# Performance work log

Measured on AMD Instinct MI355X. Metric: run time of the kernel, lower is better.

Reference implementation:

```python
import jax, jax.numpy as jnp
import numpy as np

B, S1, S2, H = 8, 2048, 2048, 1024

def setup_inputs() -> dict:
    key = jax.random.key(0)
    k1, k2, kw, kb = jax.random.split(key, 4)
    hidden1 = jax.random.normal(k1, (B, S1, H), dtype=jnp.float32)
    hidden2 = jax.random.normal(k2, (B, S2, H), dtype=jnp.float32)
    W = jax.random.normal(kw, (H, H), dtype=jnp.float32) * 0.001
    bias = jax.random.normal(kb, (1,), dtype=jnp.float32) * 0.02
    return {"hidden1": hidden1, "hidden2": hidden2, "W": W, "bias": bias}

def reference(hidden1, hidden2, W, bias):
    # weight[b, i, j] = (hidden1 @ W)[b, i, :] . hidden2[b, j, :] + bias
    weight = jnp.einsum('bih,hk,bjk->bij', hidden1, W, hidden2) + bias[0]  # (B, S1, S2)
    # softmax over s1 (dim=1), then transpose-bmm with hidden1 -> (B, S2, H)
    a1 = jax.nn.softmax(weight, axis=1)
    hidden_1 = jnp.einsum('bij,bih->bjh', a1, hidden1)
    # softmax over s2 (dim=2), bmm with hidden2 -> (B, S1, H)
    a2 = jax.nn.softmax(weight, axis=2)
    hidden_2 = jnp.einsum('bij,bjh->bih', a2, hidden2)
    return (hidden_1, hidden_2)
```

## Files before the change

kernel.cpp:

```cpp
#include <hip/hip_runtime.h>
#include <stdint.h>

#define B_  8
#define S1_ 2048
#define S2_ 2048
#define H_  1024

typedef __attribute__((ext_vector_type(8))) short bf16x8;
typedef __attribute__((ext_vector_type(4))) float f32x4;
typedef unsigned short u16;

__device__ __forceinline__ u16 f2bf(float f){
  union { float f; uint32_t v; } x; x.f = f;
  uint32_t r = x.v + 0x7fffu + ((x.v >> 16) & 1u);
  return (u16)(r >> 16);
}
__device__ __forceinline__ u16 f2h(float f){
  union { _Float16 h; u16 u; } c; c.h = (_Float16)f; return c.u;
}
__device__ __forceinline__ float h2f(u16 u){
  union { _Float16 h; u16 u; } c; c.u = u; return (float)c.h;
}
__device__ __forceinline__ uint32_t pk2bf(float lo, float hi){
  uint32_t r;
  asm("v_cvt_pk_bf16_f32 %0, %1, %2" : "=v"(r) : "v"(lo), "v"(hi));
  return r;
}
__device__ __forceinline__ void async16(void* lds, const void* g){
  __builtin_amdgcn_global_load_lds(
      (const __attribute__((address_space(1))) uint32_t*)g,
      (__attribute__((address_space(3))) uint32_t*)lds, 16, 0, 0);
}

__global__ __launch_bounds__(256) void k_cvt_bf16(const float* __restrict__ in,
                                                  u16* __restrict__ out, long n){
  long i = ((long)blockIdx.x * 256 + threadIdx.x) * 8;
  const long stride = (long)gridDim.x * 256 * 8;
  for (; i < n; i += stride){
    float4 a = *(const float4*)(in + i);
    float4 b = *(const float4*)(in + i + 4);
    union { bf16x8 v; uint32_t w[4]; } o;
    o.w[0] = pk2bf(a.x, a.y); o.w[1] = pk2bf(a.z, a.w);
    o.w[2] = pk2bf(b.x, b.y); o.w[3] = pk2bf(b.z, b.w);
    *(bf16x8*)(out + i) = o.v;
  }
}

__global__ __launch_bounds__(256) void k_tcvt(const float* __restrict__ in,
                                              u16* __restrict__ out, int R, int Cc){
  __shared__ u16 t[32][33];
  in  += (long)blockIdx.z * R * Cc;
  out += (long)blockIdx.z * R * Cc;
  const int x = threadIdx.x & 31, y0 = threadIdx.x >> 5;
  const int bx = blockIdx.x * 32, by = blockIdx.y * 32;
  for (int r = y0; r < 32; r += 8) t[r][x] = f2bf(in[(long)(by + r) * Cc + bx + x]);
  __syncthreads();
  for (int r = y0; r < 32; r += 8) out[(long)(bx + r) * R + by + x] = t[x][r];
}

__global__ __launch_bounds__(256) void k_cvtT(const float* __restrict__ in,
                                              u16* __restrict__ out_n,
                                              u16* __restrict__ out_t, int R, int Cc){
  __shared__ u16 t[32][33];
  in   += (long)blockIdx.z * R * Cc;
  out_n += (long)blockIdx.z * R * Cc;
  out_t += (long)blockIdx.z * R * Cc;
  const int x = threadIdx.x & 31, y0 = threadIdx.x >> 5;
  const int bx = blockIdx.x * 32, by = blockIdx.y * 32;
  for (int r = y0; r < 32; r += 8){
    u16 bv = f2bf(in[(long)(by + r) * Cc + bx + x]);
    out_n[(long)(by + r) * Cc + bx + x] = bv;
    t[r][x] = bv;
  }
  __syncthreads();
  for (int r = y0; r < 32; r += 8) out_t[(long)(bx + r) * R + by + x] = t[x][r];
}

template<int OM, bool STATS>
__global__ __launch_bounds__(512) void k_gemm256(
    const u16* __restrict__ A, const u16* __restrict__ Bm, void* __restrict__ Cv,
    int M, int N, int K, long sA, long sB, long sC,
    float* __restrict__ rpmax, float* __restrict__ rpsum,
    float* __restrict__ cpmax, float* __restrict__ cpsum)
{
  A += (long)blockIdx.z * sA; Bm += (long)blockIdx.z * sB;
  __shared__ u16 lds[4 * 16384];
  const int tid = threadIdx.x, lane = tid & 63, w = tid >> 6;
  const int wm = w >> 2, wn = w & 3;
  const int brow = blockIdx.x * 256, bcol = blockIdx.y * 256;

  f32x4 acc[8][4];
#pragma unroll
  for (int m=0;m<8;++m)
#pragma unroll
    for (int n=0;n<4;++n) acc[m][n] = (f32x4){0.f,0.f,0.f,0.f};

  const int fr = lane & 15;
  const int g8s = ((lane >> 4) ^ ((lane >> 1) & 3)) * 8;

  const int cc0 = w*128 + lane;
  const int cc1 = w*128 + 64 + lane;
  const int sl0 = (cc0 & 3) ^ ((cc0 >> 3) & 3);
  const int sl1 = (cc1 & 3) ^ ((cc1 >> 3) & 3);
  const u16* gA0 = A  + (long)(brow + (cc0 >> 2)) * K + sl0*8;
  const u16* gA1 = A  + (long)(brow + (cc1 >> 2)) * K + sl1*8;
  const u16* gB0 = Bm + (long)(bcol + (cc0 >> 2)) * K + sl0*8;
  const u16* gB1 = Bm + (long)(bcol + (cc1 >> 2)) * K + sl1*8;
  const int ldA0 = (w*128)*8, ldA1 = (w*128 + 64)*8;

  auto stage = [&](int buf, int t){
    u16* base = lds + buf*16384;
    async16(base + ldA0,        gA0 + t*32);
    async16(base + ldA1,        gA1 + t*32);
    async16(base + 8192 + ldA0, gB0 + t*32);
    async16(base + 8192 + ldA1, gB1 + t*32);
  };
  auto ldfrag = [&](int buf, bf16x8* a, bf16x8* b){
    const u16* At = lds + buf*16384;
    const u16* Bt = At + 8192;
#pragma unroll
    for (int n=0;n<4;++n) b[n] = *(const bf16x8*)(Bt + (wn*64 + n*16 + fr)*32 + g8s);
#pragma unroll
    for (int m=0;m<8;++m) a[m] = *(const bf16x8*)(At + (wm*128 + m*16 + fr)*32 + g8s);
  };

  const int NT = K >> 5;
  stage(0,0); stage(1,1); stage(2,2);
  asm volatile("s_waitcnt vmcnt(4)" ::: "memory");
  __builtin_amdgcn_s_barrier();

  bf16x8 a0[8], b0[4], a1[8], b1[4];
  ldfrag(0, a0, b0);

  for (int t = 0; t < NT; t += 2){
    if (t + 3 < NT) stage((t+3)&3, t+3);
    ldfrag((t+1)&3, a1, b1);
    __builtin_amdgcn_sched_barrier(0);
    __builtin_amdgcn_s_setprio(1);
#pragma unroll
    for (int m=0;m<8;++m)
#pragma unroll
      for (int n=0;n<4;++n)
        acc[m][n] = __builtin_amdgcn_mfma_f32_16x16x32_bf16(a0[m], b0[n], acc[m][n], 0,0,0);
    __builtin_amdgcn_s_setprio(0);
    asm volatile("s_waitcnt vmcnt(4)" ::: "memory");
    __builtin_amdgcn_s_barrier();

    if (t + 4 < NT) stage((t+4)&3, t+4);
    if (t + 2 < NT) ldfrag((t+2)&3, a0, b0);
    __builtin_amdgcn_sched_barrier(0);
    __builtin_amdgcn_s_setprio(1);
#pragma unroll
    for (int m=0;m<8;++m)
#pragma unroll
      for (int n=0;n<4;++n)
        acc[m][n] = __builtin_amdgcn_mfma_f32_16x16x32_bf16(a1[m], b1[n], acc[m][n], 0,0,0);
    __builtin_amdgcn_s_setprio(0);
    if (t + 2 < NT){
      asm volatile("s_waitcnt vmcnt(4)" ::: "memory");
      __builtin_amdgcn_s_barrier();
    }
  }

  const int crow = brow + wm*128 + (lane >> 4) * 4;
  const int ccol = bcol + wn*64 + fr;
  if constexpr (OM == 2){
    float* C = (float*)Cv + (long)blockIdx.z * sC;
#pragma unroll
    for (int m=0;m<8;++m)
#pragma unroll
      for (int n=0;n<4;++n){
        f32x4 v = acc[m][n];
        float* cp = C + (long)(crow + m*16) * N + ccol + n*16;
#pragma unroll
        for (int q=0;q<4;++q) cp[(long)q*N] = v[q];
      }
  } else {
    u16* C = (u16*)Cv + (long)blockIdx.z * sC;
#pragma unroll
    for (int m=0;m<8;++m)
#pragma unroll
      for (int n=0;n<4;++n){
        f32x4 v = acc[m][n];
        u16* cp = C + (long)(crow + m*16) * N + ccol + n*16;
#pragma unroll
        for (int q=0;q<4;++q) cp[(long)q*N] = OM ? f2h(v[q]) : f2bf(v[q]);
      }
  }

  if constexpr (STATS){
    const int hi = lane >> 4;
#pragma unroll
    for (int m=0;m<8;++m){
      f32x4 mx = acc[m][0];
#pragma unroll
      for (int n=1;n<4;++n)
#pragma unroll
        for (int q=0;q<4;++q) mx[q] = fmaxf(mx[q], acc[m][n][q]);
#pragma unroll
      for (int off=1; off<16; off<<=1)
#pragma unroll
        for (int q=0;q<4;++q) mx[q] = fmaxf(mx[q], __shfl_xor(mx[q], off));
      f32x4 sm = (f32x4){0.f,0.f,0.f,0.f};
#pragma unroll
      for (int n=0;n<4;++n)
#pragma unroll
        for (int q=0;q<4;++q) sm[q] += __expf(acc[m][n][q] - mx[q]);
#pragma unroll
      for (int off=1; off<16; off<<=1)
#pragma unroll
        for (int q=0;q<4;++q) sm[q] += __shfl_xor(sm[q], off);
      if (fr == 0){
        const int nb = blockIdx.y*4 + wn;
        const long rb = ((long)blockIdx.z*32 + nb)*2048 + brow + wm*128 + m*16 + hi*4;
#pragma unroll
        for (int q=0;q<4;++q){ rpmax[rb+q] = mx[q]; rpsum[rb+q] = sm[q]; }
      }
    }
#pragma unroll
    for (int n=0;n<4;++n){
      float mx = acc[0][n][0];
#pragma unroll
      for (int m=0;m<8;++m)
#pragma unroll
        for (int q=0;q<4;++q) mx = fmaxf(mx, acc[m][n][q]);
      mx = fmaxf(mx, __shfl_xor(mx, 16));
      mx = fmaxf(mx, __shfl_xor(mx, 32));
      float sm = 0.f;
#pragma unroll
      for (int m=0;m<8;++m)
#pragma unroll
        for (int q=0;q<4;++q) sm += __expf(acc[m][n][q] - mx);
      sm += __shfl_xor(sm, 16);
      sm += __shfl_xor(sm, 32);
      if (hi == 0){
        const int mb = blockIdx.x*2 + wm;
        const long cb = ((long)blockIdx.z*16 + mb)*2048 + bcol + wn*64 + n*16 + fr;
        cpmax[cb] = mx; cpsum[cb] = sm;
      }
    }
  }
}

__global__ __launch_bounds__(256) void k_combine(
    const float* __restrict__ rpmax, const float* __restrict__ rpsum,
    const float* __restrict__ cpmax, const float* __restrict__ cpsum,
    float* __restrict__ rmax, float* __restrict__ rinv,
    float* __restrict__ cmax, float* __restrict__ cinv)
{
  const long i = (long)blockIdx.x*256 + threadIdx.x;
  const int b = (int)(i >> 11), r = (int)(i & 2047);
  if (blockIdx.y == 0){
    const float* pm = rpmax + ((long)b*32)*2048 + r;
    const float* ps = rpsum + ((long)b*32)*2048 + r;
    float m = -3.4e38f;
#pragma unroll
    for (int k=0;k<32;++k) m = fmaxf(m, pm[(long)k*2048]);
    float s = 0.f;
#pragma unroll
    for (int k=0;k<32;++k) s += ps[(long)k*2048] * __expf(pm[(long)k*2048] - m);
    rmax[i] = m; rinv[i] = 1.f / s;
  } else {
    const float* pm = cpmax + ((long)b*16)*2048 + r;
    const float* ps = cpsum + ((long)b*16)*2048 + r;
    float m = -3.4e38f;
#pragma unroll
    for (int k=0;k<16;++k) m = fmaxf(m, pm[(long)k*2048]);
    float s = 0.f;
#pragma unroll
    for (int k=0;k<16;++k) s += ps[(long)k*2048] * __expf(pm[(long)k*2048] - m);
    cmax[i] = m; cinv[i] = 1.f / s;
  }
}

__global__ __launch_bounds__(256) void k_p1t(u16* __restrict__ Wg, u16* __restrict__ P2,
                                             const float* __restrict__ cmax,
                                             const float* __restrict__ cinv,
                                             const float* __restrict__ rmax,
                                             const float* __restrict__ rinv){
  const int ti = blockIdx.x, tj = blockIdx.y;
  if (tj < ti) return;
  const int b = blockIdx.z;
  u16* S = Wg + (long)b * S1_ * S2_;
  const int jl = threadIdx.x & 63, ig = threadIdx.x >> 6;
  const int I0 = ti*64, J0 = tj*64;
  const float cmA = cmax[b*S2_ + J0 + jl], ciA = cinv[b*S2_ + J0 + jl];
  const float cmB = cmax[b*S2_ + I0 + jl], ciB = cinv[b*S2_ + I0 + jl];
  float ra[16], rc[16];
#pragma unroll
  for (int q=0;q<16;++q) ra[q] = h2f(S[(long)(I0 + ig*16 + q)*S2_ + J0 + jl]);
#pragma unroll
  for (int q=0;q<16;++q) rc[q] = h2f(S[(long)(J0 + ig*16 + q)*S2_ + I0 + jl]);

  if (P2){
    u16* P2b = P2 + (long)b * S1_ * S2_;
#pragma unroll
    for (int q=0;q<16;++q){
      const int r = I0 + ig*16 + q;
      P2b[(long)r*S2_ + J0 + jl] = f2bf(__expf(ra[q] - rmax[b*S1_+r]) * rinv[b*S1_+r]);
    }
    if (ti != tj){
#pragma unroll
      for (int q=0;q<16;++q){
        const int r = J0 + ig*16 + q;
        P2b[(long)r*S2_ + I0 + jl] = f2bf(__expf(rc[q] - rmax[b*S1_+r]) * rinv[b*S1_+r]);
      }
    }
  }

  float a[16], c[16];
#pragma unroll
  for (int q=0;q<16;++q) a[q] = __expf(ra[q] - cmA) * ciA;
#pragma unroll
  for (int q=0;q<16;++q) c[q] = __expf(rc[q] - cmB) * ciB;
  __syncthreads();
  union { bf16x8 v; uint32_t w4[4]; } o0, o1;
#pragma unroll
  for (int k=0;k<4;++k){ o0.w4[k] = pk2bf(a[2*k], a[2*k+1]); o1.w4[k] = pk2bf(a[8+2*k], a[9+2*k]); }
  *(bf16x8*)(S + (long)(J0+jl)*S2_ + I0 + ig*16)     = o0.v;
  *(bf16x8*)(S + (long)(J0+jl)*S2_ + I0 + ig*16 + 8) = o1.v;
#pragma unroll
  for (int k=0;k<4;++k){ o0.w4[k] = pk2bf(c[2*k], c[2*k+1]); o1.w4[k] = pk2bf(c[8+2*k], c[9+2*k]); }
  *(bf16x8*)(S + (long)(I0+jl)*S2_ + J0 + ig*16)     = o0.v;
  *(bf16x8*)(S + (long)(I0+jl)*S2_ + J0 + ig*16 + 8) = o1.v;
}

__global__ __launch_bounds__(256) void k_gemm_h2(
    const u16* __restrict__ Wg, const u16* __restrict__ Bt, float* __restrict__ C,
    const float* __restrict__ rmax, const float* __restrict__ rinv)
{
  const int b = blockIdx.z;
  const u16* A  = Wg + (long)b * S1_ * S2_;
  const u16* Bp = Bt + (long)b * H_ * S2_;
  float* Cp = C + (long)b * S1_ * H_;

  __shared__ u16 As[128*32];
  __shared__ u16 Bs[128*32];
  const int tid = threadIdx.x, lane = tid & 63, w = tid >> 6;
  const int wr = (w >> 1) * 64, wc = (w & 1) * 64;
  const int brow = blockIdx.x * 128, bcol = blockIdx.y * 128;
  f32x4 acc[4][4];
#pragma unroll
  for (int m=0;m<4;++m)
#pragma unroll
    for (int n=0;n<4;++n) acc[m][n] = (f32x4){0.f,0.f,0.f,0.f};

  const int arow = w*16 + (lane >> 2);
  const int scol = (lane & 3) * 8;
  const u16* gA0 = A + (long)(brow + arow) * S2_ + scol;
  const u16* gA1 = gA0 + (long)64 * S2_;
  const float rm0 = rmax[b*S1_ + brow + arow],      ri0 = rinv[b*S1_ + brow + arow];
  const float rm1 = rmax[b*S1_ + brow + arow + 64], ri1 = rinv[b*S1_ + brow + arow + 64];
  u16* wA0 = As + arow*32 + scol;
  u16* wA1 = As + (arow+64)*32 + scol;

  const u16* gb = Bp + (long)(bcol + arow) * S2_ + scol;
  u16* lB0 = Bs + (w*16)*32;  u16* lB1 = Bs + (64 + w*16)*32;

  const int koff = (lane >> 4) * 8;
  const int fr = lane & 15;

  for (int k0 = 0; k0 < S2_; k0 += 32){
    bf16x8 x0 = *(const bf16x8*)(gA0 + k0);
    bf16x8 x1 = *(const bf16x8*)(gA1 + k0);
    async16(lB0, gb);  async16(lB1, gb + (long)64*S2_);
    gb += 32;
    union { bf16x8 v; uint32_t w4[4]; } y0, y1;
#pragma unroll
    for (int k=0;k<4;++k){
      y0.w4[k] = pk2bf(__expf(h2f((u16)x0[2*k])   - rm0) * ri0,
                       __expf(h2f((u16)x0[2*k+1]) - rm0) * ri0);
      y1.w4[k] = pk2bf(__expf(h2f((u16)x1[2*k])   - rm1) * ri1,
                       __expf(h2f((u16)x1[2*k+1]) - rm1) * ri1);
    }
    *(bf16x8*)wA0 = y0.v;
    *(bf16x8*)wA1 = y1.v;
    __syncthreads();
    bf16x8 af[4], bf[4];
#pragma unroll
    for (int m=0;m<4;++m) af[m] = *(const bf16x8*)(As + (wr + m*16 + fr)*32 + koff);
#pragma unroll
    for (int n=0;n<4;++n) bf[n] = *(const bf16x8*)(Bs + (wc + n*16 + fr)*32 + koff);
#pragma unroll
    for (int m=0;m<4;++m)
#pragma unroll
      for (int n=0;n<4;++n)
        acc[m][n] = __builtin_amdgcn_mfma_f32_16x16x32_bf16(af[m], bf[n], acc[m][n], 0,0,0);
    __syncthreads();
  }
  const int crow = brow + wr + (lane >> 4) * 4;
  const int ccol = bcol + wc + fr;
#pragma unroll
  for (int m=0;m<4;++m)
#pragma unroll
    for (int n=0;n<4;++n){
      f32x4 v = acc[m][n];
      float* cp = Cp + (long)(crow + m*16) * H_ + ccol + n*16;
#pragma unroll
      for (int q=0;q<4;++q) cp[(long)q*H_] = v[q];
    }
}

extern "C" void kernel_launch(void* const* d_in, const int* in_sizes, int n_in,
                              void* d_out, int out_size, void* d_ws, size_t ws_size,
                              hipStream_t stream)
{
  const float* h1 = (const float*)d_in[0];
  const float* h2 = (const float*)d_in[1];
  const float* W  = (const float*)d_in[2];
  float* out0 = (float*)d_out;
  float* out1 = out0 + (size_t)B_ * S2_ * H_;

  const long NE = (long)B_ * S1_ * H_;
  const long NS = (long)B_ * S1_ * S2_;

  char* ws = (char*)d_ws;
  size_t off = 0;
  float* rmax = (float*)(ws + off); off += (size_t)B_*S1_*4;
  float* rinv = (float*)(ws + off); off += (size_t)B_*S1_*4;
  float* cmax = (float*)(ws + off); off += (size_t)B_*S2_*4;
  float* cinv = (float*)(ws + off); off += (size_t)B_*S2_*4;
  u16* Wg  = (u16*)(ws + off);
  u16* WTb = Wg;
  off += (size_t)NS*2;
  u16* h1t = (u16*)(ws + off); off += (size_t)NE*2;

  const bool use_p2 = ws_size >= off + (size_t)NS*2;
  u16* P2 = use_p2 ? (u16*)(ws + off) : (u16*)nullptr;
  size_t off2 = off + (use_p2 ? (size_t)NS*2 : 0);
  const bool ws_h2t = ws_size >= off2 + (size_t)NE*2;

  u16* h1b = (u16*)out0;
  u16* h2b = (u16*)out0 + NE;
  u16* h2t = ws_h2t ? (u16*)(ws + off2) : (u16*)out0;
  u16* Qb  = (u16*)out1;
  float* rpmax = (float*)((u16*)out1 + NE);
  float* rpsum = rpmax + (size_t)B_*32*2048;
  float* cpmax = rpsum + (size_t)B_*32*2048;
  float* cpsum = cpmax + (size_t)B_*16*2048;

  k_cvtT<<<dim3(32,64,8), 256, 0, stream>>>(h1, h1b, h1t, S1_, H_);
  if (ws_h2t){
    k_cvtT<<<dim3(32,64,8), 256, 0, stream>>>(h2, h2b, h2t, S2_, H_);
  } else {
    k_cvt_bf16<<<dim3(4096), 256, 0, stream>>>(h2, h2b, NE);
  }
  k_tcvt<<<dim3(32,32,1), 256, 0, stream>>>(W, WTb, H_, H_);
  k_gemm256<0,false><<<dim3(8, 4, 8), 512, 0, stream>>>(h1b, WTb, Qb, S1_, H_, H_,
        (long)S1_*H_, 0L, (long)S1_*H_, nullptr, nullptr, nullptr, nullptr);
  if (!ws_h2t){
    k_tcvt<<<dim3(32,64,8), 256, 0, stream>>>(h2, h2t, S2_, H_);
  }
  k_gemm256<1,true><<<dim3(8, 8, 8), 512, 0, stream>>>(Qb, h2b, Wg, S1_, S2_, H_,
        (long)S1_*H_, (long)S2_*H_, (long)S1_*S2_, rpmax, rpsum, cpmax, cpsum);
  k_combine<<<dim3(64, 2), 256, 0, stream>>>(rpmax, rpsum, cpmax, cpsum,
                                             rmax, rinv, cmax, cinv);
  if (use_p2){
    k_p1t<<<dim3(32,32,8), 256, 0, stream>>>(Wg, P2, cmax, cinv, rmax, rinv);
    k_gemm256<2,false><<<dim3(8, 4, 8), 512, 0, stream>>>(P2, h2t, out1, S1_, H_, S2_,
          (long)S1_*S2_, (long)H_*S2_, (long)S1_*H_, nullptr, nullptr, nullptr, nullptr);
  } else {
    k_gemm_h2<<<dim3(16, 8, 8), 256, 0, stream>>>(Wg, h2t, out1, rmax, rinv);
    k_p1t<<<dim3(32,32,8), 256, 0, stream>>>(Wg, (u16*)nullptr, cmax, cinv, rmax, rinv);
  }
  k_gemm256<2,false><<<dim3(8, 4, 8), 512, 0, stream>>>(Wg, h1t, out0, S2_, H_, S1_,
        (long)S1_*S2_, (long)H_*S1_, (long)S2_*H_, nullptr, nullptr, nullptr, nullptr);
}
```

Before: 410.5 us.

## Vectorize convert-transpose kernel and swizzle GEMM block order across XCDs

The fp32-to-bf16 convert-and-transpose kernel now works on 64x64 tiles with float4 loads and ushort4 stores in place of scalar 32x32 accesses, which cuts the number of memory instructions. The GEMM kernel remaps its linear block id so that consecutive hardware-dispatched blocks (round-robined across the 8 XCDs) land on contiguous tiles. This is meant to improve L2 locality per XCD. It costs some extra integer divide and modulo work per block, and the 68-wide LDS row padding may still cause bank conflicts on the column reads.

```diff
diff --git a/kernel.cpp b/kernel.cpp
--- a/kernel.cpp
+++ b/kernel.cpp
@@ -58,22 +58,35 @@
   for (int r = y0; r < 32; r += 8) out[(long)(bx + r) * R + by + x] = t[x][r];
 }
 
-__global__ __launch_bounds__(256) void k_cvtT(const float* __restrict__ in,
-                                              u16* __restrict__ out_n,
-                                              u16* __restrict__ out_t, int R, int Cc){
-  __shared__ u16 t[32][33];
-  in   += (long)blockIdx.z * R * Cc;
+__global__ __launch_bounds__(256) void k_cvtT2(const float* __restrict__ in,
+                                               u16* __restrict__ out_n,
+                                               u16* __restrict__ out_t, int R, int Cc){
+  __shared__ u16 t[64][68];
+  in    += (long)blockIdx.z * R * Cc;
   out_n += (long)blockIdx.z * R * Cc;
   out_t += (long)blockIdx.z * R * Cc;
-  const int x = threadIdx.x & 31, y0 = threadIdx.x >> 5;
-  const int bx = blockIdx.x * 32, by = blockIdx.y * 32;
-  for (int r = y0; r < 32; r += 8){
-    u16 bv = f2bf(in[(long)(by + r) * Cc + bx + x]);
-    out_n[(long)(by + r) * Cc + bx + x] = bv;
-    t[r][x] = bv;
+  const int tid = threadIdx.x;
+  const int r0 = tid >> 4;
+  const int c4 = (tid & 15) * 4;
+  const int bx = blockIdx.x * 64;
+  const int by = blockIdx.y * 64;
+#pragma unroll
+  for (int it = 0; it < 4; ++it){
+    const int r = it*16 + r0;
+    float4 v = *(const float4*)(in + (long)(by + r)*Cc + bx + c4);
+    u16 b0 = f2bf(v.x), b1 = f2bf(v.y), b2 = f2bf(v.z), b3 = f2bf(v.w);
+    ushort4 o; o.x = b0; o.y = b1; o.z = b2; o.w = b3;
+    *(ushort4*)(out_n + (long)(by + r)*Cc + bx + c4) = o;
+    t[r][c4] = b0; t[r][c4+1] = b1; t[r][c4+2] = b2; t[r][c4+3] = b3;
   }
   __syncthreads();
-  for (int r = y0; r < 32; r += 8) out_t[(long)(bx + r) * R + by + x] = t[x][r];
+#pragma unroll
+  for (int it = 0; it < 4; ++it){
+    const int c = it*16 + r0;
+    ushort4 o;
+    o.x = t[c4  ][c]; o.y = t[c4+1][c]; o.z = t[c4+2][c]; o.w = t[c4+3][c];
+    *(ushort4*)(out_t + (long)(bx + c)*R + by + c4) = o;
+  }
 }
 
 template<int OM, bool STATS>
@@ -83,11 +96,21 @@
     float* __restrict__ rpmax, float* __restrict__ rpsum,
     float* __restrict__ cpmax, float* __restrict__ cpsum)
 {
-  A += (long)blockIdx.z * sA; Bm += (long)blockIdx.z * sB;
+  const int GX = gridDim.x, GY = gridDim.y;
+  const long plane = (long)GX * GY;
+  const long tot = plane * gridDim.z;
+  const long lin = blockIdx.x + (long)GX * (blockIdx.y + (long)GY * blockIdx.z);
+  const long chunk = tot >> 3;
+  const long swz = (lin & 7) * chunk + (lin >> 3);
+  const int bz = (int)(swz / plane);
+  const int rr = (int)(swz % plane);
+  const int by_ = rr / GX, bx_ = rr % GX;
+
+  A += (long)bz * sA; Bm += (long)bz * sB;
   __shared__ u16 lds[4 * 16384];
   const int tid = threadIdx.x, lane = tid & 63, w = tid >> 6;
   const int wm = w >> 2, wn = w & 3;
-  const int brow = blockIdx.x * 256, bcol = blockIdx.y * 256;
+  const int brow = bx_ * 256, bcol = by_ * 256;
 
   f32x4 acc[8][4];
 #pragma unroll
@@ -165,7 +188,7 @@
   const int crow = brow + wm*128 + (lane >> 4) * 4;
   const int ccol = bcol + wn*64 + fr;
   if constexpr (OM == 2){
-    float* C = (float*)Cv + (long)blockIdx.z * sC;
+    float* C = (float*)Cv + (long)bz * sC;
 #pragma unroll
     for (int m=0;m<8;++m)
 #pragma unroll
@@ -176,7 +199,7 @@
         for (int q=0;q<4;++q) cp[(long)q*N] = v[q];
       }
   } else {
-    u16* C = (u16*)Cv + (long)blockIdx.z * sC;
+    u16* C = (u16*)Cv + (long)bz * sC;
 #pragma unroll
     for (int m=0;m<8;++m)
 #pragma unroll
@@ -211,8 +234,8 @@
 #pragma unroll
         for (int q=0;q<4;++q) sm[q] += __shfl_xor(sm[q], off);
       if (fr == 0){
-        const int nb = blockIdx.y*4 + wn;
-        const long rb = ((long)blockIdx.z*32 + nb)*2048 + brow + wm*128 + m*16 + hi*4;
+        const int nb = by_*4 + wn;
+        const long rb = ((long)bz*32 + nb)*2048 + brow + wm*128 + m*16 + hi*4;
 #pragma unroll
         for (int q=0;q<4;++q){ rpmax[rb+q] = mx[q]; rpsum[rb+q] = sm[q]; }
       }
@@ -234,8 +257,8 @@
       sm += __shfl_xor(sm, 16);
       sm += __shfl_xor(sm, 32);
       if (hi == 0){
-        const int mb = blockIdx.x*2 + wm;
-        const long cb = ((long)blockIdx.z*16 + mb)*2048 + bcol + wn*64 + n*16 + fr;
+        const int mb = bx_*2 + wm;
+        const long cb = ((long)bz*16 + mb)*2048 + bcol + wn*64 + n*16 + fr;
         cpmax[cb] = mx; cpsum[cb] = sm;
       }
     }
@@ -439,9 +462,9 @@
   float* cpmax = rpsum + (size_t)B_*32*2048;
   float* cpsum = cpmax + (size_t)B_*16*2048;
 
-  k_cvtT<<<dim3(32,64,8), 256, 0, stream>>>(h1, h1b, h1t, S1_, H_);
+  k_cvtT2<<<dim3(16,32,8), 256, 0, stream>>>(h1, h1b, h1t, S1_, H_);
   if (ws_h2t){
-    k_cvtT<<<dim3(32,64,8), 256, 0, stream>>>(h2, h2b, h2t, S2_, H_);
+    k_cvtT2<<<dim3(16,32,8), 256, 0, stream>>>(h2, h2b, h2t, S2_, H_);
   } else {
     k_cvt_bf16<<<dim3(4096), 256, 0, stream>>>(h2, h2b, NE);
   }
```

Measured after the change: 385.1 us (median of 2 runs). 6.2% less time.
